# Kernel optimization log

Measured on AMD Instinct MI355X. Metric: run time of the kernel, lower is better.

## Reference

```python
import jax, jax.numpy as jnp
import numpy as np

N = 100000
E = 1600000
IN_DIM, HID, Z = 128, 64, 32


def gcn_conv(x, src, dst, num_nodes, W, b):
    """PyG GCNConv: add self-loops, symmetric deg^-1/2 normalization.
    x: [N, F_in]; src/dst: [E] int (self-loops already appended by caller wrapper).
    """
    h = x @ W  # [N, F_out] transform first (PyG order)
    ones = jnp.ones(src.shape[0], dtype=x.dtype)
    deg = jax.ops.segment_sum(ones, dst, num_segments=num_nodes)  # in-degree incl. self-loop
    dinv = jnp.where(deg > 0, jax.lax.rsqrt(deg), 0.0)
    norm = dinv[src] * dinv[dst]  # [E]
    msgs = h[src] * norm[:, None]  # [E, F_out] irregular gather
    out = jax.ops.segment_sum(msgs, dst, num_segments=num_nodes)  # scatter-add
    return out + b


def setup_inputs() -> dict:
    key = jax.random.key(0)
    ks = jax.random.split(key, 10)
    x = jax.random.normal(ks[0], (N, IN_DIM), dtype=jnp.float32)
    edge_index = jax.random.randint(ks[1], (2, E), 0, N, dtype=jnp.int64)

    def glorot(k, fan_in, fan_out):
        s = jnp.sqrt(6.0 / (fan_in + fan_out))
        return jax.random.uniform(k, (fan_in, fan_out), jnp.float32, -s, s)

    return {
        "x": x,
        "edge_index": edge_index,
        "W1": glorot(ks[2], IN_DIM, HID),
        "b1": jnp.zeros((HID,), jnp.float32),
        "W2": glorot(ks[3], HID, Z),
        "b2": jnp.zeros((Z,), jnp.float32),
        "Wmu": glorot(ks[4], Z, Z),
        "bmu": jnp.zeros((Z,), jnp.float32),
        "Wlv": glorot(ks[5], Z, Z),
        "blv": jnp.zeros((Z,), jnp.float32),
    }


def reference(x, edge_index, W1, b1, W2, b2, Wmu, bmu, Wlv, blv):
    num_nodes = x.shape[0]
    loop = jnp.arange(num_nodes, dtype=edge_index.dtype)
    src = jnp.concatenate([edge_index[0], loop])  # self-loops appended
    dst = jnp.concatenate([edge_index[1], loop])
    h = jax.nn.relu(gcn_conv(x, src, dst, num_nodes, W1, b1))
    h = gcn_conv(h, src, dst, num_nodes, W2, b2)
    mu = h @ Wmu + bmu
    logvar = h @ Wlv + blv
    return (mu, logvar)
```

## Files before the change

kernel.cpp:

```cpp
#include <hip/hip_runtime.h>

#define N_NODES 100000
#define N_EDGES 1600000
#define IN_F   128
#define HID_F  64
#define Z_F    32
#define NBUK   782
#define BCAP   3072
#define P1T    4096
#define P1_BLOCKS ((N_EDGES + P1T - 1) / P1T)
#define AGG_CAP 2048
#define G1_BLOCKS ((N_NODES + 63) / 64)

typedef unsigned int uint32;
typedef __attribute__((ext_vector_type(8))) short bf16x8;
typedef __attribute__((ext_vector_type(4))) float f32x4;

__device__ __forceinline__ unsigned short f2bf(float f) {
    unsigned u = __float_as_uint(f);
    u = (u + 0x7FFF + ((u >> 16) & 1)) >> 16;
    return (unsigned short)u;
}
__device__ __forceinline__ uint32 pack2bf(float lo, float hi) {
    return (uint32)f2bf(lo) | ((uint32)f2bf(hi) << 16);
}
__device__ __forceinline__ float bflo(uint32 u) { return __uint_as_float(u << 16); }
__device__ __forceinline__ float bfhi(uint32 u) { return __uint_as_float(u & 0xFFFF0000u); }

#define ACC8(u) { a0 += bflo(u.x); a1 += bfhi(u.x); a2 += bflo(u.y); a3 += bfhi(u.y); \
                  a4 += bflo(u.z); a5 += bfhi(u.z); a6 += bflo(u.w); a7 += bfhi(u.w); }

__global__ __launch_bounds__(512) void phase1_kernel(const int* __restrict__ ei,
                                                     int* __restrict__ gcur,
                                                     uint32* __restrict__ pairs,
                                                     const float* __restrict__ W1,
                                                     const float* __restrict__ W2,
                                                     const float* __restrict__ Wmu,
                                                     const float* __restrict__ Wlv,
                                                     unsigned short* __restrict__ Wt1,
                                                     unsigned short* __restrict__ Wt2,
                                                     unsigned short* __restrict__ Wth) {
    if (blockIdx.x == P1_BLOCKS) {
        int t = threadIdx.x;
        for (int i = t; i < IN_F * HID_F; i += 512) {
            int n = i >> 7, k = i & 127;
            Wt1[i] = f2bf(W1[k * HID_F + n]);
        }
        for (int i = t; i < HID_F * Z_F; i += 512) {
            int n = i >> 6, k = i & 63;
            Wt2[i] = f2bf(W2[k * Z_F + n]);
        }
        for (int i = t; i < Z_F * 64; i += 512) {
            int n = i >> 5, k = i & 31;
            Wth[i] = f2bf(n < 32 ? Wmu[k * Z_F + n] : Wlv[k * Z_F + (n - 32)]);
        }
        return;
    }
    __shared__ int hist[NBUK];
    __shared__ int lbase[NBUK];
    __shared__ int gbase[NBUK];
    __shared__ int lcur[NBUK];
    __shared__ uint32 stage[P1T];
    __shared__ unsigned short sbid[P1T];
    __shared__ int part[512];
    int tid = threadIdx.x;
    int e0 = blockIdx.x * P1T;
    int ecnt = N_EDGES - e0; if (ecnt > P1T) ecnt = P1T;
    for (int b = tid; b < NBUK; b += 512) { hist[b] = 0; lcur[b] = 0; }
    __syncthreads();
    int myd[8];
#pragma unroll
    for (int i = 0; i < 8; i++) {
        int k = tid + i * 512;
        myd[i] = (k < ecnt) ? ei[N_EDGES + e0 + k] : -1;
    }
#pragma unroll
    for (int i = 0; i < 8; i++)
        if (myd[i] >= 0) atomicAdd(&hist[myd[i] >> 7], 1);
    __syncthreads();
    int t2 = tid * 2;
    int l0 = 0, l1 = 0, s = 0;
    if (t2 + 0 < NBUK) { l0 = hist[t2 + 0]; s += l0; }
    if (t2 + 1 < NBUK) { l1 = hist[t2 + 1]; s += l1; }
    part[tid] = s;
    __syncthreads();
    for (int off = 1; off < 512; off <<= 1) {
        int add = (tid >= off) ? part[tid - off] : 0;
        __syncthreads();
        part[tid] += add;
        __syncthreads();
    }
    int run = part[tid] - s;
    if (t2 + 0 < NBUK) { lbase[t2 + 0] = run; run += l0; }
    if (t2 + 1 < NBUK) { lbase[t2 + 1] = run; }
    for (int b = tid; b < NBUK; b += 512) {
        int h = hist[b];
        gbase[b] = h ? atomicAdd(&gcur[b], h) : 0;
    }
    __syncthreads();
#pragma unroll
    for (int i = 0; i < 8; i++) {
        int k = tid + i * 512;
        if (k < ecnt) {
            int sN = ei[e0 + k];
            int d  = myd[i];
            int b = d >> 7;
            int slot = lbase[b] + atomicAdd(&lcur[b], 1);
            stage[slot] = (uint32)sN | ((uint32)(d & 127) << 17);
            sbid[slot] = (unsigned short)b;
        }
    }
    __syncthreads();
    for (int k = tid; k < ecnt; k += 512) {
        int b = sbid[k];
        int r = gbase[b] + (k - lbase[k < ecnt ? b : 0]);
        r = gbase[b] + (k - lbase[b]);
        if (r < BCAP) pairs[(size_t)b * BCAP + r] = stage[k];
    }
}

__global__ __launch_bounds__(256) void p2g1_kernel(const uint32* __restrict__ pairs,
                                                   const int* __restrict__ gcur,
                                                   int* __restrict__ rowptr,
                                                   float* __restrict__ dinv,
                                                   int* __restrict__ col,
                                                   const float* __restrict__ x,
                                                   const unsigned short* __restrict__ Wt1,
                                                   unsigned short* __restrict__ t1) {
    int tid = threadIdx.x;
    if (blockIdx.x < NBUK) {
        __shared__ int lhist[128];
        __shared__ int lscan[128];
        __shared__ int lcur[128];
        __shared__ int stage[BCAP];
        __shared__ int wsum[4];
        int b = blockIdx.x;
        int cnt_b = gcur[b];
        if (cnt_b > BCAP) cnt_b = BCAP;
        int partial = 0;
        for (int i = tid; i < b; i += 256) partial += gcur[i];
#pragma unroll
        for (int off = 32; off > 0; off >>= 1) partial += __shfl_down(partial, off);
        if (tid < 128) { lhist[tid] = 0; lcur[tid] = 0; }
        if ((tid & 63) == 0) wsum[tid >> 6] = partial;
        __syncthreads();
        int gbase = wsum[0] + wsum[1] + wsum[2] + wsum[3];
        int node0 = b << 7;
        int nb = N_NODES - node0;
        if (nb > 128) nb = 128;
        const uint32* pb = pairs + (size_t)b * BCAP;
        for (int k = tid; k < cnt_b; k += 256) atomicAdd(&lhist[pb[k] >> 17], 1);
        __syncthreads();
        int v = (tid < 128) ? lhist[tid] : 0;
        if (tid < 128) lscan[tid] = v;
        __syncthreads();
        for (int off = 1; off < 128; off <<= 1) {
            int add = (tid < 128 && tid >= off) ? lscan[tid - off] : 0;
            __syncthreads();
            if (tid < 128) lscan[tid] += add;
            __syncthreads();
        }
        if (tid < 128) lscan[tid] -= v;
        __syncthreads();
        if (tid < nb) {
            rowptr[node0 + tid] = gbase + lscan[tid];
            dinv[node0 + tid] = rsqrtf((float)(lhist[tid] + 1));
        }
        if (b == NBUK - 1 && tid == 0) rowptr[N_NODES] = N_EDGES;
        for (int k = tid; k < cnt_b; k += 256) {
            uint32 u = pb[k];
            int ld = u >> 17;
            int r = atomicAdd(&lcur[ld], 1);
            stage[lscan[ld] + r] = (int)(u & 0x1FFFF);
        }
        __syncthreads();
        for (int k = tid; k < cnt_b; k += 256) col[gbase + k] = stage[k];
        return;
    }
    __shared__ unsigned short Cs[64 * 72];
    __shared__ float dv[64];
    __shared__ int h64[64];
    int g = blockIdx.x - NBUK;
    int node0 = g * 64;
    int bk = node0 >> 7, half = (node0 >> 6) & 1;
    int cnt_b = gcur[bk];
    if (cnt_b > BCAP) cnt_b = BCAP;
    if (tid < 64) h64[tid] = 0;
    __syncthreads();
    const uint32* pb = pairs + (size_t)bk * BCAP;
    for (int k = tid; k < cnt_b; k += 256) {
        int ld = pb[k] >> 17;
        if ((ld >> 6) == half) atomicAdd(&h64[ld & 63], 1);
    }
    __syncthreads();
    if (tid < 64) {
        int n = node0 + tid;
        dv[tid] = (n < N_NODES) ? rsqrtf((float)(h64[tid] + 1)) : 0.f;
    }
    __syncthreads();
    int w = tid >> 6, lane = tid & 63;
    int m = lane & 15, quad = lane >> 4;
    int row = w * 16 + m;
    int node = node0 + row;
    const float* xr = x + (size_t)min(node, N_NODES - 1) * IN_F;
    f32x4 acc0 = {0.f, 0.f, 0.f, 0.f};
    f32x4 acc1 = acc0, acc2 = acc0, acc3 = acc0;
#pragma unroll
    for (int ks = 0; ks < 4; ks++) {
        int kb = ks * 32 + quad * 8;
        float4 f0 = *(const float4*)(xr + kb);
        float4 f1 = *(const float4*)(xr + kb + 4);
        union { bf16x8 v; unsigned short u[8]; } A;
        A.u[0] = f2bf(f0.x); A.u[1] = f2bf(f0.y); A.u[2] = f2bf(f0.z); A.u[3] = f2bf(f0.w);
        A.u[4] = f2bf(f1.x); A.u[5] = f2bf(f1.y); A.u[6] = f2bf(f1.z); A.u[7] = f2bf(f1.w);
        bf16x8 b0 = *(const bf16x8*)&Wt1[(0 * 16 + m) * IN_F + kb];
        bf16x8 b1 = *(const bf16x8*)&Wt1[(1 * 16 + m) * IN_F + kb];
        bf16x8 b2 = *(const bf16x8*)&Wt1[(2 * 16 + m) * IN_F + kb];
        bf16x8 b3 = *(const bf16x8*)&Wt1[(3 * 16 + m) * IN_F + kb];
        acc0 = __builtin_amdgcn_mfma_f32_16x16x32_bf16(A.v, b0, acc0, 0, 0, 0);
        acc1 = __builtin_amdgcn_mfma_f32_16x16x32_bf16(A.v, b1, acc1, 0, 0, 0);
        acc2 = __builtin_amdgcn_mfma_f32_16x16x32_bf16(A.v, b2, acc2, 0, 0, 0);
        acc3 = __builtin_amdgcn_mfma_f32_16x16x32_bf16(A.v, b3, acc3, 0, 0, 0);
    }
    int rbase = w * 16 + quad * 4;
#pragma unroll
    for (int reg = 0; reg < 4; reg++) {
        int r = rbase + reg;
        float d = dv[r];
        Cs[r * 72 +  0 + m] = f2bf(acc0[reg] * d);
        Cs[r * 72 + 16 + m] = f2bf(acc1[reg] * d);
        Cs[r * 72 + 32 + m] = f2bf(acc2[reg] * d);
        Cs[r * 72 + 48 + m] = f2bf(acc3[reg] * d);
    }
    __syncthreads();
#pragma unroll
    for (int it = 0; it < 4; it++) {
        int idx = it * 256 + tid;
        int r = idx >> 4, c = idx & 15;
        int nd = node0 + r;
        if (nd < N_NODES) {
            uint2 vv = *(const uint2*)&Cs[r * 72 + c * 4];
            *(uint2*)&t1[(size_t)nd * HID_F + c * 4] = vv;
        }
    }
}

__global__ __launch_bounds__(256) void agg1gemm2_kernel(const unsigned short* __restrict__ t1,
                                                        const int* __restrict__ rowptr,
                                                        const int* __restrict__ col,
                                                        const float* __restrict__ dinv,
                                                        const float* __restrict__ b1,
                                                        const unsigned short* __restrict__ Wt2,
                                                        unsigned short* __restrict__ t2s) {
    __shared__ int lcol[AGG_CAP];
    __shared__ int lrp[65];
    __shared__ float ldv[64];
    __shared__ unsigned short h1s[64 * 72];
    __shared__ unsigned short Cs[64 * 36];
    int tid = threadIdx.x;
    int node0 = blockIdx.x * 64;
    if (tid < 65) lrp[tid] = rowptr[min(node0 + tid, N_NODES)];
    __syncthreads();
    int s0 = lrp[0];
    int cnt = lrp[64] - s0; if (cnt > AGG_CAP) cnt = AGG_CAP;
    for (int k = tid; k < cnt; k += 256) lcol[k] = col[s0 + k];
    if (tid < 64) {
        int n = node0 + tid;
        ldv[tid] = (n < N_NODES) ? dinv[n] : 0.f;
    }
    __syncthreads();
    int lane = tid & 63, w = tid >> 6;
    int grp = lane >> 3, fl = lane & 7;
    int gg = w * 8 + grp;
    const uint4* t1q = (const uint4*)t1;
    float4 bb0 = ((const float4*)b1)[fl * 2];
    float4 bb1 = ((const float4*)b1)[fl * 2 + 1];
#pragma unroll
    for (int rep = 0; rep < 2; rep++) {
        int li = gg + rep * 32;
        int node = node0 + li;
        uint4 pk = make_uint4(0u, 0u, 0u, 0u);
        if (node < N_NODES) {
            int s = lrp[li] - s0;
            int e = lrp[li + 1] - s0; if (e > cnt) e = cnt;
            float a0 = 0.f, a1 = 0.f, a2 = 0.f, a3 = 0.f;
            float a4 = 0.f, a5 = 0.f, a6 = 0.f, a7 = 0.f;
            int p = s;
            for (; p + 3 < e; p += 4) {
                int c0 = lcol[p], c1 = lcol[p + 1], c2 = lcol[p + 2], c3 = lcol[p + 3];
                uint4 u0 = t1q[(size_t)c0 * 8 + fl];
                uint4 u1 = t1q[(size_t)c1 * 8 + fl];
                uint4 u2 = t1q[(size_t)c2 * 8 + fl];
                uint4 u3 = t1q[(size_t)c3 * 8 + fl];
                ACC8(u0); ACC8(u1); ACC8(u2); ACC8(u3);
            }
            for (; p < e; p++) {
                uint4 u = t1q[(size_t)lcol[p] * 8 + fl];
                ACC8(u);
            }
            uint4 us = t1q[(size_t)node * 8 + fl];
            float di = ldv[li];
            float o0 = fmaxf(di * (a0 + bflo(us.x)) + bb0.x, 0.f);
            float o1 = fmaxf(di * (a1 + bfhi(us.x)) + bb0.y, 0.f);
            float o2 = fmaxf(di * (a2 + bflo(us.y)) + bb0.z, 0.f);
            float o3 = fmaxf(di * (a3 + bfhi(us.y)) + bb0.w, 0.f);
            float o4 = fmaxf(di * (a4 + bflo(us.z)) + bb1.x, 0.f);
            float o5 = fmaxf(di * (a5 + bfhi(us.z)) + bb1.y, 0.f);
            float o6 = fmaxf(di * (a6 + bflo(us.w)) + bb1.z, 0.f);
            float o7 = fmaxf(di * (a7 + bfhi(us.w)) + bb1.w, 0.f);
            pk.x = pack2bf(o0, o1);
            pk.y = pack2bf(o2, o3);
            pk.z = pack2bf(o4, o5);
            pk.w = pack2bf(o6, o7);
        }
        *(uint4*)&h1s[li * 72 + fl * 8] = pk;
    }
    __syncthreads();
    int m = lane & 15, quad = lane >> 4;
    int row = w * 16 + m;
    f32x4 acc0 = {0.f, 0.f, 0.f, 0.f};
    f32x4 acc1 = acc0;
#pragma unroll
    for (int ks = 0; ks < 2; ks++) {
        int kb = ks * 32 + quad * 8;
        bf16x8 a  = *(const bf16x8*)&h1s[row * 72 + kb];
        bf16x8 b0 = *(const bf16x8*)&Wt2[(0 * 16 + m) * HID_F + kb];
        bf16x8 b1v = *(const bf16x8*)&Wt2[(1 * 16 + m) * HID_F + kb];
        acc0 = __builtin_amdgcn_mfma_f32_16x16x32_bf16(a, b0, acc0, 0, 0, 0);
        acc1 = __builtin_amdgcn_mfma_f32_16x16x32_bf16(a, b1v, acc1, 0, 0, 0);
    }
    int rbase = w * 16 + quad * 4;
#pragma unroll
    for (int reg = 0; reg < 4; reg++) {
        int r = rbase + reg;
        float d = ldv[r];
        Cs[r * 36 +  0 + m] = f2bf(acc0[reg] * d);
        Cs[r * 36 + 16 + m] = f2bf(acc1[reg] * d);
    }
    __syncthreads();
#pragma unroll
    for (int it = 0; it < 2; it++) {
        int idx = it * 256 + tid;
        int r = idx >> 3, c = idx & 7;
        int nd = node0 + r;
        if (nd < N_NODES) {
            uint2 vv = *(const uint2*)&Cs[r * 36 + c * 4];
            *(uint2*)&t2s[(size_t)nd * Z_F + c * 4] = vv;
        }
    }
}

__global__ __launch_bounds__(256) void agg2heads_kernel(const unsigned short* __restrict__ t2s,
                                                        const int* __restrict__ rowptr,
                                                        const int* __restrict__ col,
                                                        const float* __restrict__ dinv,
                                                        const float* __restrict__ b2,
                                                        const unsigned short* __restrict__ Wth,
                                                        const float* __restrict__ bmu,
                                                        const float* __restrict__ blv,
                                                        float* __restrict__ out) {
    __shared__ int lcol[AGG_CAP];
    __shared__ int lrp[65];
    __shared__ float ldv[64];
    __shared__ unsigned short h2s[64 * 40];
    __shared__ float Cf[64 * 68];
    __shared__ float bias[64];
    int tid = threadIdx.x;
    int node0 = blockIdx.x * 64;
    if (tid < 65) lrp[tid] = rowptr[min(node0 + tid, N_NODES)];
    else if (tid >= 96 && tid < 128) bias[tid - 96] = bmu[tid - 96];
    else if (tid >= 128 && tid < 160) bias[tid - 96] = blv[tid - 128];
    __syncthreads();
    int s0 = lrp[0];
    int cnt = lrp[64] - s0; if (cnt > AGG_CAP) cnt = AGG_CAP;
    for (int k = tid; k < cnt; k += 256) lcol[k] = col[s0 + k];
    if (tid < 64) {
        int n = node0 + tid;
        ldv[tid] = (n < N_NODES) ? dinv[n] : 0.f;
    }
    __syncthreads();
    int lane = tid & 63, w = tid >> 6;
    int grp = lane >> 2, fo = lane & 3;
    int li = w * 16 + grp;
    const uint4* t2q = (const uint4*)t2s;
    float4 bb0 = ((const float4*)b2)[fo * 2];
    float4 bb1 = ((const float4*)b2)[fo * 2 + 1];
    {
        int node = node0 + li;
        uint4 pk = make_uint4(0u, 0u, 0u, 0u);
        if (node < N_NODES) {
            int s = lrp[li] - s0;
            int e = lrp[li + 1] - s0; if (e > cnt) e = cnt;
            float a0 = 0.f, a1 = 0.f, a2 = 0.f, a3 = 0.f;
            float a4 = 0.f, a5 = 0.f, a6 = 0.f, a7 = 0.f;
            int p = s;
            for (; p + 3 < e; p += 4) {
                int c0 = lcol[p], c1 = lcol[p + 1], c2 = lcol[p + 2], c3 = lcol[p + 3];
                uint4 u0 = t2q[(size_t)c0 * 4 + fo];
                uint4 u1 = t2q[(size_t)c1 * 4 + fo];
                uint4 u2 = t2q[(size_t)c2 * 4 + fo];
                uint4 u3 = t2q[(size_t)c3 * 4 + fo];
                ACC8(u0); ACC8(u1); ACC8(u2); ACC8(u3);
            }
            for (; p < e; p++) {
                uint4 u = t2q[(size_t)lcol[p] * 4 + fo];
                ACC8(u);
            }
            uint4 us = t2q[(size_t)node * 4 + fo];
            float di = ldv[li];
            float o0 = di * (a0 + bflo(us.x)) + bb0.x;
            float o1 = di * (a1 + bfhi(us.x)) + bb0.y;
            float o2 = di * (a2 + bflo(us.y)) + bb0.z;
            float o3 = di * (a3 + bfhi(us.y)) + bb0.w;
            float o4 = di * (a4 + bflo(us.z)) + bb1.x;
            float o5 = di * (a5 + bfhi(us.z)) + bb1.y;
            float o6 = di * (a6 + bflo(us.w)) + bb1.z;
            float o7 = di * (a7 + bfhi(us.w)) + bb1.w;
            pk.x = pack2bf(o0, o1);
            pk.y = pack2bf(o2, o3);
            pk.z = pack2bf(o4, o5);
            pk.w = pack2bf(o6, o7);
        }
        *(uint4*)&h2s[li * 40 + fo * 8] = pk;
    }
    __syncthreads();
    int m = lane & 15, quad = lane >> 4;
    int row = w * 16 + m;
    int kb = quad * 8;
    bf16x8 a  = *(const bf16x8*)&h2s[row * 40 + kb];
    bf16x8 b0 = *(const bf16x8*)&Wth[(0 * 16 + m) * Z_F + kb];
    bf16x8 b1 = *(const bf16x8*)&Wth[(1 * 16 + m) * Z_F + kb];
    bf16x8 b2v = *(const bf16x8*)&Wth[(2 * 16 + m) * Z_F + kb];
    bf16x8 b3 = *(const bf16x8*)&Wth[(3 * 16 + m) * Z_F + kb];
    f32x4 acc0 = {0.f, 0.f, 0.f, 0.f};
    f32x4 acc1 = acc0, acc2 = acc0, acc3 = acc0;
    acc0 = __builtin_amdgcn_mfma_f32_16x16x32_bf16(a, b0, acc0, 0, 0, 0);
    acc1 = __builtin_amdgcn_mfma_f32_16x16x32_bf16(a, b1, acc1, 0, 0, 0);
    acc2 = __builtin_amdgcn_mfma_f32_16x16x32_bf16(a, b2v, acc2, 0, 0, 0);
    acc3 = __builtin_amdgcn_mfma_f32_16x16x32_bf16(a, b3, acc3, 0, 0, 0);
    int rbase = w * 16 + quad * 4;
#pragma unroll
    for (int reg = 0; reg < 4; reg++) {
        int r = rbase + reg;
        Cf[r * 68 +  0 + m] = acc0[reg] + bias[ 0 + m];
        Cf[r * 68 + 16 + m] = acc1[reg] + bias[16 + m];
        Cf[r * 68 + 32 + m] = acc2[reg] + bias[32 + m];
        Cf[r * 68 + 48 + m] = acc3[reg] + bias[48 + m];
    }
    __syncthreads();
#pragma unroll
    for (int it = 0; it < 2; it++) {
        int idx = it * 256 + tid;
        int r = idx >> 3, c = idx & 7;
        int nd = node0 + r;
        if (nd < N_NODES) {
            float4 vmu = *(const float4*)&Cf[r * 68 + c * 4];
            float4 vlv = *(const float4*)&Cf[r * 68 + 32 + c * 4];
            *(float4*)&out[(size_t)nd * Z_F + c * 4] = vmu;
            *(float4*)&out[(size_t)N_NODES * Z_F + (size_t)nd * Z_F + c * 4] = vlv;
        }
    }
}

extern "C" void kernel_launch(void* const* d_in, const int* in_sizes, int n_in,
                              void* d_out, int out_size, void* d_ws, size_t ws_size,
                              hipStream_t stream) {
    const float* x   = (const float*)d_in[0];
    const int*   ei  = (const int*)d_in[1];
    const float* W1  = (const float*)d_in[2];
    const float* b1  = (const float*)d_in[3];
    const float* W2  = (const float*)d_in[4];
    const float* b2  = (const float*)d_in[5];
    const float* Wmu = (const float*)d_in[6];
    const float* bmu = (const float*)d_in[7];
    const float* Wlv = (const float*)d_in[8];
    const float* blv = (const float*)d_in[9];
    float* out = (float*)d_out;

    char* ws = (char*)d_ws;
    size_t off = 0;
    auto A = [&](size_t bytes) {
        size_t r = off;
        off += (bytes + 255) & ~(size_t)255;
        return r;
    };
    int*   gcur   = (int*)(ws + A((size_t)NBUK * 4));
    int*   rowptr = (int*)(ws + A((size_t)(N_NODES + 1) * 4));
    float* dinv   = (float*)(ws + A((size_t)N_NODES * 4));
    unsigned short* Wt1 = (unsigned short*)(ws + A((size_t)IN_F * HID_F * 2));
    unsigned short* Wt2 = (unsigned short*)(ws + A((size_t)HID_F * Z_F * 2));
    unsigned short* Wth = (unsigned short*)(ws + A((size_t)Z_F * 64 * 2));
    int*   col        = (int*)(ws + A((size_t)N_EDGES * 4));
    char*  reg1 = ws + A((size_t)NBUK * BCAP * 4);
    uint32* pairs = (uint32*)reg1;
    unsigned short* t2s = (unsigned short*)reg1;
    unsigned short* t1 = (unsigned short*)(ws + A((size_t)N_NODES * HID_F * 2));

    hipMemsetAsync(gcur, 0, (size_t)NBUK * 4, stream);

    phase1_kernel<<<P1_BLOCKS + 1, 512, 0, stream>>>(ei, gcur, pairs,
                                                     W1, W2, Wmu, Wlv, Wt1, Wt2, Wth);
    p2g1_kernel<<<NBUK + G1_BLOCKS, 256, 0, stream>>>(pairs, gcur, rowptr, dinv, col,
                                                      x, Wt1, t1);
    agg1gemm2_kernel<<<G1_BLOCKS, 256, 0, stream>>>(t1, rowptr, col, dinv, b1, Wt2, t2s);
    agg2heads_kernel<<<G1_BLOCKS, 256, 0, stream>>>(t2s, rowptr, col, dinv, b2, Wth, bmu, blv, out);
}
```

Measured before the change: 210.6 us.

## Fuse bucketing with GEMM1, drop CSR build, aggregate directly from bucket pairs

```diff
diff --git a/kernel.cpp b/kernel.cpp
--- a/kernel.cpp
+++ b/kernel.cpp
@@ -9,8 +9,7 @@
 #define BCAP   3072
 #define P1T    4096
 #define P1_BLOCKS ((N_EDGES + P1T - 1) / P1T)
-#define AGG_CAP 2048
-#define G1_BLOCKS ((N_NODES + 63) / 64)
+#define DEG_PAD 100352
 
 typedef unsigned int uint32;
 typedef __attribute__((ext_vector_type(8))) short bf16x8;
@@ -29,175 +28,109 @@
 
 #define ACC8(u) { a0 += bflo(u.x); a1 += bfhi(u.x); a2 += bflo(u.y); a3 += bfhi(u.y); \
                   a4 += bflo(u.z); a5 += bfhi(u.z); a6 += bflo(u.w); a7 += bfhi(u.w); }
-
-__global__ __launch_bounds__(512) void phase1_kernel(const int* __restrict__ ei,
-                                                     int* __restrict__ gcur,
-                                                     uint32* __restrict__ pairs,
-                                                     const float* __restrict__ W1,
-                                                     const float* __restrict__ W2,
-                                                     const float* __restrict__ Wmu,
-                                                     const float* __restrict__ Wlv,
-                                                     unsigned short* __restrict__ Wt1,
-                                                     unsigned short* __restrict__ Wt2,
-                                                     unsigned short* __restrict__ Wth) {
+#define FMA8(r,u) { a0 = fmaf(r, bflo(u.x), a0); a1 = fmaf(r, bfhi(u.x), a1); \
+                    a2 = fmaf(r, bflo(u.y), a2); a3 = fmaf(r, bfhi(u.y), a3); \
+                    a4 = fmaf(r, bflo(u.z), a4); a5 = fmaf(r, bfhi(u.z), a5); \
+                    a6 = fmaf(r, bflo(u.w), a6); a7 = fmaf(r, bfhi(u.w), a7); }
+
+__global__ __launch_bounds__(512) void k1_kernel(const int* __restrict__ ei,
+                                                 int* __restrict__ gcur,
+                                                 uint32* __restrict__ pairs,
+                                                 int* __restrict__ deg,
+                                                 const float* __restrict__ W1,
+                                                 const float* __restrict__ W2,
+                                                 const float* __restrict__ Wmu,
+                                                 const float* __restrict__ Wlv,
+                                                 unsigned short* __restrict__ Wt2,
+                                                 unsigned short* __restrict__ Wth,
+                                                 const float* __restrict__ x,
+                                                 unsigned short* __restrict__ t1u) {
+    __shared__ __align__(16) int arena[9784];
+    int tid = threadIdx.x;
     if (blockIdx.x == P1_BLOCKS) {
-        int t = threadIdx.x;
-        for (int i = t; i < IN_F * HID_F; i += 512) {
-            int n = i >> 7, k = i & 127;
-            Wt1[i] = f2bf(W1[k * HID_F + n]);
-        }
-        for (int i = t; i < HID_F * Z_F; i += 512) {
+        for (int i = tid; i < HID_F * Z_F; i += 512) {
             int n = i >> 6, k = i & 63;
             Wt2[i] = f2bf(W2[k * Z_F + n]);
         }
-        for (int i = t; i < Z_F * 64; i += 512) {
+        for (int i = tid; i < Z_F * 64; i += 512) {
             int n = i >> 5, k = i & 31;
             Wth[i] = f2bf(n < 32 ? Wmu[k * Z_F + n] : Wlv[k * Z_F + (n - 32)]);
         }
         return;
     }
-    __shared__ int hist[NBUK];
-    __shared__ int lbase[NBUK];
-    __shared__ int gbase[NBUK];
-    __shared__ int lcur[NBUK];
-    __shared__ uint32 stage[P1T];
-    __shared__ unsigned short sbid[P1T];
-    __shared__ int part[512];
-    int tid = threadIdx.x;
-    int e0 = blockIdx.x * P1T;
-    int ecnt = N_EDGES - e0; if (ecnt > P1T) ecnt = P1T;
-    for (int b = tid; b < NBUK; b += 512) { hist[b] = 0; lcur[b] = 0; }
-    __syncthreads();
-    int myd[8];
-#pragma unroll
-    for (int i = 0; i < 8; i++) {
-        int k = tid + i * 512;
-        myd[i] = (k < ecnt) ? ei[N_EDGES + e0 + k] : -1;
-    }
-#pragma unroll
-    for (int i = 0; i < 8; i++)
-        if (myd[i] >= 0) atomicAdd(&hist[myd[i] >> 7], 1);
-    __syncthreads();
-    int t2 = tid * 2;
-    int l0 = 0, l1 = 0, s = 0;
-    if (t2 + 0 < NBUK) { l0 = hist[t2 + 0]; s += l0; }
-    if (t2 + 1 < NBUK) { l1 = hist[t2 + 1]; s += l1; }
-    part[tid] = s;
-    __syncthreads();
-    for (int off = 1; off < 512; off <<= 1) {
-        int add = (tid >= off) ? part[tid - off] : 0;
-        __syncthreads();
-        part[tid] += add;
-        __syncthreads();
-    }
-    int run = part[tid] - s;
-    if (t2 + 0 < NBUK) { lbase[t2 + 0] = run; run += l0; }
-    if (t2 + 1 < NBUK) { lbase[t2 + 1] = run; }
-    for (int b = tid; b < NBUK; b += 512) {
-        int h = hist[b];
-        gbase[b] = h ? atomicAdd(&gcur[b], h) : 0;
-    }
-    __syncthreads();
-#pragma unroll
-    for (int i = 0; i < 8; i++) {
-        int k = tid + i * 512;
-        if (k < ecnt) {
-            int sN = ei[e0 + k];
-            int d  = myd[i];
-            int b = d >> 7;
-            int slot = lbase[b] + atomicAdd(&lcur[b], 1);
-            stage[slot] = (uint32)sN | ((uint32)(d & 127) << 17);
-            sbid[slot] = (unsigned short)b;
-        }
-    }
-    __syncthreads();
-    for (int k = tid; k < ecnt; k += 512) {
-        int b = sbid[k];
-        int r = gbase[b] + (k - lbase[k < ecnt ? b : 0]);
-        r = gbase[b] + (k - lbase[b]);
-        if (r < BCAP) pairs[(size_t)b * BCAP + r] = stage[k];
-    }
-}
-
-__global__ __launch_bounds__(256) void p2g1_kernel(const uint32* __restrict__ pairs,
-                                                   const int* __restrict__ gcur,
-                                                   int* __restrict__ rowptr,
-                                                   float* __restrict__ dinv,
-                                                   int* __restrict__ col,
-                                                   const float* __restrict__ x,
-                                                   const unsigned short* __restrict__ Wt1,
-                                                   unsigned short* __restrict__ t1) {
-    int tid = threadIdx.x;
-    if (blockIdx.x < NBUK) {
-        __shared__ int lhist[128];
-        __shared__ int lscan[128];
-        __shared__ int lcur[128];
-        __shared__ int stage[BCAP];
-        __shared__ int wsum[4];
-        int b = blockIdx.x;
-        int cnt_b = gcur[b];
-        if (cnt_b > BCAP) cnt_b = BCAP;
-        int partial = 0;
-        for (int i = tid; i < b; i += 256) partial += gcur[i];
-#pragma unroll
-        for (int off = 32; off > 0; off >>= 1) partial += __shfl_down(partial, off);
-        if (tid < 128) { lhist[tid] = 0; lcur[tid] = 0; }
-        if ((tid & 63) == 0) wsum[tid >> 6] = partial;
-        __syncthreads();
-        int gbase = wsum[0] + wsum[1] + wsum[2] + wsum[3];
-        int node0 = b << 7;
-        int nb = N_NODES - node0;
-        if (nb > 128) nb = 128;
-        const uint32* pb = pairs + (size_t)b * BCAP;
-        for (int k = tid; k < cnt_b; k += 256) atomicAdd(&lhist[pb[k] >> 17], 1);
-        __syncthreads();
-        int v = (tid < 128) ? lhist[tid] : 0;
-        if (tid < 128) lscan[tid] = v;
-        __syncthreads();
-        for (int off = 1; off < 128; off <<= 1) {
-            int add = (tid < 128 && tid >= off) ? lscan[tid - off] : 0;
+    if (blockIdx.x < P1_BLOCKS) {
+        int* hist  = arena;
+        int* lbase = arena + NBUK;
+        int* gbase = arena + 2 * NBUK;
+        int* lcur  = arena + 3 * NBUK;
+        int* part  = arena + 4 * NBUK;
+        uint32* stage = (uint32*)(arena + 4 * NBUK + 512);
+        unsigned short* sbid = (unsigned short*)(arena + 4 * NBUK + 512 + P1T);
+        int e0 = blockIdx.x * P1T;
+        int ecnt = N_EDGES - e0; if (ecnt > P1T) ecnt = P1T;
+        for (int b = tid; b < NBUK; b += 512) { hist[b] = 0; lcur[b] = 0; }
+        __syncthreads();
+        int myd[8];
+#pragma unroll
+        for (int i = 0; i < 8; i++) {
+            int k = tid + i * 512;
+            myd[i] = (k < ecnt) ? ei[N_EDGES + e0 + k] : -1;
+        }
+#pragma unroll
+        for (int i = 0; i < 8; i++)
+            if (myd[i] >= 0) {
+                atomicAdd(&hist[myd[i] >> 7], 1);
+                atomicAdd(&deg[myd[i]], 1);
+            }
+        __syncthreads();
+        int t2 = tid * 2;
+        int l0 = 0, l1 = 0, s = 0;
+        if (t2 + 0 < NBUK) { l0 = hist[t2 + 0]; s += l0; }
+        if (t2 + 1 < NBUK) { l1 = hist[t2 + 1]; s += l1; }
+        part[tid] = s;
+        __syncthreads();
+        for (int off = 1; off < 512; off <<= 1) {
+            int add = (tid >= off) ? part[tid - off] : 0;
             __syncthreads();
-            if (tid < 128) lscan[tid] += add;
+            part[tid] += add;
             __syncthreads();
         }
-        if (tid < 128) lscan[tid] -= v;
-        __syncthreads();
-        if (tid < nb) {
-            rowptr[node0 + tid] = gbase + lscan[tid];
-            dinv[node0 + tid] = rsqrtf((float)(lhist[tid] + 1));
-        }
-        if (b == NBUK - 1 && tid == 0) rowptr[N_NODES] = N_EDGES;
-        for (int k = tid; k < cnt_b; k += 256) {
-            uint32 u = pb[k];
-            int ld = u >> 17;
-            int r = atomicAdd(&lcur[ld], 1);
-            stage[lscan[ld] + r] = (int)(u & 0x1FFFF);
-        }
-        __syncthreads();
-        for (int k = tid; k < cnt_b; k += 256) col[gbase + k] = stage[k];
+        int run = part[tid] - s;
+        if (t2 + 0 < NBUK) { lbase[t2 + 0] = run; run += l0; }
+        if (t2 + 1 < NBUK) { lbase[t2 + 1] = run; }
+        for (int b = tid; b < NBUK; b += 512) {
+            int h = hist[b];
+            gbase[b] = h ? atomicAdd(&gcur[b], h) : 0;
+        }
+        __syncthreads();
+#pragma unroll
+        for (int i = 0; i < 8; i++) {
+            int k = tid + i * 512;
+            if (k < ecnt) {
+                int sN = ei[e0 + k];
+                int d  = myd[i];
+                int b = d >> 7;
+                int slot = lbase[b] + atomicAdd(&lcur[b], 1);
+                stage[slot] = (uint32)sN | ((uint32)(d & 127) << 17);
+                sbid[slot] = (unsigned short)b;
+            }
+        }
+        __syncthreads();
+        for (int k = tid; k < ecnt; k += 512) {
+            int b = sbid[k];
+            int r = gbase[b] + (k - lbase[b]);
+            if (r < BCAP) pairs[(size_t)b * BCAP + r] = stage[k];
+        }
         return;
     }
-    __shared__ unsigned short Cs[64 * 72];
-    __shared__ float dv[64];
-    __shared__ int h64[64];
-    int g = blockIdx.x - NBUK;
-    int node0 = g * 64;
-    int bk = node0 >> 7, half = (node0 >> 6) & 1;
-    int cnt_b = gcur[bk];
-    if (cnt_b > BCAP) cnt_b = BCAP;
-    if (tid < 64) h64[tid] = 0;
-    __syncthreads();
-    const uint32* pb = pairs + (size_t)bk * BCAP;
-    for (int k = tid; k < cnt_b; k += 256) {
-        int ld = pb[k] >> 17;
-        if ((ld >> 6) == half) atomicAdd(&h64[ld & 63], 1);
-    }
-    __syncthreads();
-    if (tid < 64) {
-        int n = node0 + tid;
-        dv[tid] = (n < N_NODES) ? rsqrtf((float)(h64[tid] + 1)) : 0.f;
-    }
-    __syncthreads();
+    unsigned short* Cs   = (unsigned short*)arena;
+    unsigned short* Wt1s = (unsigned short*)(arena + 4608);
+    for (int i = tid; i < IN_F * HID_F; i += 512) {
+        int k = i >> 6, n = i & 63;
+        Wt1s[n * 132 + k] = f2bf(W1[i]);
+    }
+    __syncthreads();
+    int node0 = (blockIdx.x - P1_BLOCKS - 1) * 128;
     int w = tid >> 6, lane = tid & 63;
     int m = lane & 15, quad = lane >> 4;
     int row = w * 16 + m;
@@ -213,10 +146,10 @@
         union { bf16x8 v; unsigned short u[8]; } A;
         A.u[0] = f2bf(f0.x); A.u[1] = f2bf(f0.y); A.u[2] = f2bf(f0.z); A.u[3] = f2bf(f0.w);
         A.u[4] = f2bf(f1.x); A.u[5] = f2bf(f1.y); A.u[6] = f2bf(f1.z); A.u[7] = f2bf(f1.w);
-        bf16x8 b0 = *(const bf16x8*)&Wt1[(0 * 16 + m) * IN_F + kb];
-        bf16x8 b1 = *(const bf16x8*)&Wt1[(1 * 16 + m) * IN_F + kb];
-        bf16x8 b2 = *(const bf16x8*)&Wt1[(2 * 16 + m) * IN_F + kb];
-        bf16x8 b3 = *(const bf16x8*)&Wt1[(3 * 16 + m) * IN_F + kb];
+        bf16x8 b0 = *(const bf16x8*)&Wt1s[(0 * 16 + m) * 132 + kb];
+        bf16x8 b1 = *(const bf16x8*)&Wt1s[(1 * 16 + m) * 132 + kb];
+        bf16x8 b2 = *(const bf16x8*)&Wt1s[(2 * 16 + m) * 132 + kb];
+        bf16x8 b3 = *(const bf16x8*)&Wt1s[(3 * 16 + m) * 132 + kb];
         acc0 = __builtin_amdgcn_mfma_f32_16x16x32_bf16(A.v, b0, acc0, 0, 0, 0);
         acc1 = __builtin_amdgcn_mfma_f32_16x16x32_bf16(A.v, b1, acc1, 0, 0, 0);
         acc2 = __builtin_amdgcn_mfma_f32_16x16x32_bf16(A.v, b2, acc2, 0, 0, 0);
@@ -226,63 +159,81 @@
 #pragma unroll
     for (int reg = 0; reg < 4; reg++) {
         int r = rbase + reg;
-        float d = dv[r];
-        Cs[r * 72 +  0 + m] = f2bf(acc0[reg] * d);
-        Cs[r * 72 + 16 + m] = f2bf(acc1[reg] * d);
-        Cs[r * 72 + 32 + m] = f2bf(acc2[reg] * d);
-        Cs[r * 72 + 48 + m] = f2bf(acc3[reg] * d);
+        Cs[r * 72 +  0 + m] = f2bf(acc0[reg]);
+        Cs[r * 72 + 16 + m] = f2bf(acc1[reg]);
+        Cs[r * 72 + 32 + m] = f2bf(acc2[reg]);
+        Cs[r * 72 + 48 + m] = f2bf(acc3[reg]);
     }
     __syncthreads();
 #pragma unroll
     for (int it = 0; it < 4; it++) {
-        int idx = it * 256 + tid;
+        int idx = it * 512 + tid;
         int r = idx >> 4, c = idx & 15;
         int nd = node0 + r;
         if (nd < N_NODES) {
             uint2 vv = *(const uint2*)&Cs[r * 72 + c * 4];
-            *(uint2*)&t1[(size_t)nd * HID_F + c * 4] = vv;
-        }
-    }
-}
-
-__global__ __launch_bounds__(256) void agg1gemm2_kernel(const unsigned short* __restrict__ t1,
-                                                        const int* __restrict__ rowptr,
-                                                        const int* __restrict__ col,
-                                                        const float* __restrict__ dinv,
+            *(uint2*)&t1u[(size_t)nd * HID_F + c * 4] = vv;
+        }
+    }
+}
+
+__global__ __launch_bounds__(512) void agg1gemm2_kernel(const unsigned short* __restrict__ t1u,
+                                                        const uint32* __restrict__ pairs,
+                                                        const int* __restrict__ gcur,
+                                                        const int* __restrict__ deg,
                                                         const float* __restrict__ b1,
                                                         const unsigned short* __restrict__ Wt2,
                                                         unsigned short* __restrict__ t2s) {
-    __shared__ int lcol[AGG_CAP];
-    __shared__ int lrp[65];
-    __shared__ float ldv[64];
-    __shared__ unsigned short h1s[64 * 72];
-    __shared__ unsigned short Cs[64 * 36];
+    __shared__ __align__(16) int arena[BCAP + 128 * 72 / 2];
+    __shared__ int lhist[128];
+    __shared__ int lscan[128];
+    __shared__ int lcur[128];
+    __shared__ float dv[128];
+    int* lcol = arena;
+    unsigned short* h1s = (unsigned short*)(arena + BCAP);
+    unsigned short* Cs  = (unsigned short*)arena;
     int tid = threadIdx.x;
-    int node0 = blockIdx.x * 64;
-    if (tid < 65) lrp[tid] = rowptr[min(node0 + tid, N_NODES)];
-    __syncthreads();
-    int s0 = lrp[0];
-    int cnt = lrp[64] - s0; if (cnt > AGG_CAP) cnt = AGG_CAP;
-    for (int k = tid; k < cnt; k += 256) lcol[k] = col[s0 + k];
-    if (tid < 64) {
-        int n = node0 + tid;
-        ldv[tid] = (n < N_NODES) ? dinv[n] : 0.f;
+    int b = blockIdx.x;
+    int node0 = b << 7;
+    int cnt = gcur[b]; if (cnt > BCAP) cnt = BCAP;
+    const uint32* pb = pairs + (size_t)b * BCAP;
+    if (tid < 128) { lhist[tid] = 0; lcur[tid] = 0; }
+    __syncthreads();
+    for (int k = tid; k < cnt; k += 512) atomicAdd(&lhist[pb[k] >> 17], 1);
+    __syncthreads();
+    int v = (tid < 128) ? lhist[tid] : 0;
+    if (tid < 128) lscan[tid] = v;
+    __syncthreads();
+    for (int off = 1; off < 128; off <<= 1) {
+        int add = (tid < 128 && tid >= off) ? lscan[tid - off] : 0;
+        __syncthreads();
+        if (tid < 128) lscan[tid] += add;
+        __syncthreads();
+    }
+    if (tid < 128) lscan[tid] -= v;
+    __syncthreads();
+    if (tid < 128) dv[tid] = (node0 + tid < N_NODES) ? rsqrtf((float)(lhist[tid] + 1)) : 0.f;
+    for (int k = tid; k < cnt; k += 512) {
+        uint32 u = pb[k];
+        int ld = u >> 17;
+        int r = atomicAdd(&lcur[ld], 1);
+        lcol[lscan[ld] + r] = (int)(u & 0x1FFFF);
     }
     __syncthreads();
     int lane = tid & 63, w = tid >> 6;
     int grp = lane >> 3, fl = lane & 7;
     int gg = w * 8 + grp;
-    const uint4* t1q = (const uint4*)t1;
+    const uint4* t1q = (const uint4*)t1u;
     float4 bb0 = ((const float4*)b1)[fl * 2];
     float4 bb1 = ((const float4*)b1)[fl * 2 + 1];
 #pragma unroll
     for (int rep = 0; rep < 2; rep++) {
-        int li = gg + rep * 32;
+        int li = gg + rep * 64;
         int node = node0 + li;
         uint4 pk = make_uint4(0u, 0u, 0u, 0u);
         if (node < N_NODES) {
-            int s = lrp[li] - s0;
-            int e = lrp[li + 1] - s0; if (e > cnt) e = cnt;
+            int s = lscan[li];
+            int e = s + lhist[li];
             float a0 = 0.f, a1 = 0.f, a2 = 0.f, a3 = 0.f;
             float a4 = 0.f, a5 = 0.f, a6 = 0.f, a7 = 0.f;
             int p = s;
@@ -292,22 +243,29 @@
                 uint4 u1 = t1q[(size_t)c1 * 8 + fl];
                 uint4 u2 = t1q[(size_t)c2 * 8 + fl];
                 uint4 u3 = t1q[(size_t)c3 * 8 + fl];
-                ACC8(u0); ACC8(u1); ACC8(u2); ACC8(u3);
+                int d0 = deg[c0], d1 = deg[c1], d2 = deg[c2], d3 = deg[c3];
+                float r0 = rsqrtf((float)(d0 + 1));
+                float r1 = rsqrtf((float)(d1 + 1));
+                float r2 = rsqrtf((float)(d2 + 1));
+                float r3 = rsqrtf((float)(d3 + 1));
+                FMA8(r0, u0); FMA8(r1, u1); FMA8(r2, u2); FMA8(r3, u3);
             }
             for (; p < e; p++) {
-                uint4 u = t1q[(size_t)lcol[p] * 8 + fl];
-                ACC8(u);
+                int c = lcol[p];
+                uint4 u = t1q[(size_t)c * 8 + fl];
+                float r = rsqrtf((float)(deg[c] + 1));
+                FMA8(r, u);
             }
             uint4 us = t1q[(size_t)node * 8 + fl];
-            float di = ldv[li];
-            float o0 = fmaxf(di * (a0 + bflo(us.x)) + bb0.x, 0.f);
-            float o1 = fmaxf(di * (a1 + bfhi(us.x)) + bb0.y, 0.f);
-            float o2 = fmaxf(di * (a2 + bflo(us.y)) + bb0.z, 0.f);
-            float o3 = fmaxf(di * (a3 + bfhi(us.y)) + bb0.w, 0.f);
-            float o4 = fmaxf(di * (a4 + bflo(us.z)) + bb1.x, 0.f);
-            float o5 = fmaxf(di * (a5 + bfhi(us.z)) + bb1.y, 0.f);
-            float o6 = fmaxf(di * (a6 + bflo(us.w)) + bb1.z, 0.f);
-            float o7 = fmaxf(di * (a7 + bfhi(us.w)) + bb1.w, 0.f);
+            float dvl = dv[li];
+            float o0 = fmaxf(fmaf(dvl, fmaf(dvl, bflo(us.x), a0), bb0.x), 0.f);
+            float o1 = fmaxf(fmaf(dvl, fmaf(dvl, bfhi(us.x), a1), bb0.y), 0.f);
+            float o2 = fmaxf(fmaf(dvl, fmaf(dvl, bflo(us.y), a2), bb0.z), 0.f);
+            float o3 = fmaxf(fmaf(dvl, fmaf(dvl, bfhi(us.y), a3), bb0.w), 0.f);
+            float o4 = fmaxf(fmaf(dvl, fmaf(dvl, bflo(us.z), a4), bb1.x), 0.f);
+            float o5 = fmaxf(fmaf(dvl, fmaf(dvl, bfhi(us.z), a5), bb1.y), 0.f);
+            float o6 = fmaxf(fmaf(dvl, fmaf(dvl, bflo(us.w), a6), bb1.z), 0.f);
+            float o7 = fmaxf(fmaf(dvl, fmaf(dvl, bfhi(us.w), a7), bb1.w), 0.f);
             pk.x = pack2bf(o0, o1);
             pk.y = pack2bf(o2, o3);
             pk.z = pack2bf(o4, o5);
@@ -324,23 +282,23 @@
     for (int ks = 0; ks < 2; ks++) {
         int kb = ks * 32 + quad * 8;
         bf16x8 a  = *(const bf16x8*)&h1s[row * 72 + kb];
-        bf16x8 b0 = *(const bf16x8*)&Wt2[(0 * 16 + m) * HID_F + kb];
-        bf16x8 b1v = *(const bf16x8*)&Wt2[(1 * 16 + m) * HID_F + kb];
-        acc0 = __builtin_amdgcn_mfma_f32_16x16x32_bf16(a, b0, acc0, 0, 0, 0);
-        acc1 = __builtin_amdgcn_mfma_f32_16x16x32_bf16(a, b1v, acc1, 0, 0, 0);
+        bf16x8 B0 = *(const bf16x8*)&Wt2[(0 * 16 + m) * HID_F + kb];
+        bf16x8 B1 = *(const bf16x8*)&Wt2[(1 * 16 + m) * HID_F + kb];
+        acc0 = __builtin_amdgcn_mfma_f32_16x16x32_bf16(a, B0, acc0, 0, 0, 0);
+        acc1 = __builtin_amdgcn_mfma_f32_16x16x32_bf16(a, B1, acc1, 0, 0, 0);
     }
     int rbase = w * 16 + quad * 4;
 #pragma unroll
     for (int reg = 0; reg < 4; reg++) {
         int r = rbase + reg;
-        float d = ldv[r];
+        float d = dv[r];
         Cs[r * 36 +  0 + m] = f2bf(acc0[reg] * d);
         Cs[r * 36 + 16 + m] = f2bf(acc1[reg] * d);
     }
     __syncthreads();
 #pragma unroll
     for (int it = 0; it < 2; it++) {
-        int idx = it * 256 + tid;
+        int idx = it * 512 + tid;
         int r = idx >> 3, c = idx & 7;
         int nd = node0 + r;
         if (nd < N_NODES) {
@@ -350,33 +308,51 @@
     }
 }
 
-__global__ __launch_bounds__(256) void agg2heads_kernel(const unsigned short* __restrict__ t2s,
-                                                        const int* __restrict__ rowptr,
-                                                        const int* __restrict__ col,
-                                                        const float* __restrict__ dinv,
+__global__ __launch_bounds__(512) void agg2heads_kernel(const unsigned short* __restrict__ t2s,
+                                                        const uint32* __restrict__ pairs,
+                                                        const int* __restrict__ gcur,
                                                         const float* __restrict__ b2,
                                                         const unsigned short* __restrict__ Wth,
                                                         const float* __restrict__ bmu,
                                                         const float* __restrict__ blv,
                                                         float* __restrict__ out) {
-    __shared__ int lcol[AGG_CAP];
-    __shared__ int lrp[65];
-    __shared__ float ldv[64];
-    __shared__ unsigned short h2s[64 * 40];
-    __shared__ float Cf[64 * 68];
+    __shared__ __align__(16) int arena[BCAP + 128 * 40 / 2];
+    __shared__ int lhist[128];
+    __shared__ int lscan[128];
+    __shared__ int lcur[128];
+    __shared__ float dv[128];
     __shared__ float bias[64];
+    int* lcol = arena;
+    unsigned short* h2s = (unsigned short*)(arena + BCAP);
+    float* Cf = (float*)arena;
     int tid = threadIdx.x;
-    int node0 = blockIdx.x * 64;
-    if (tid < 65) lrp[tid] = rowptr[min(node0 + tid, N_NODES)];
-    else if (tid >= 96 && tid < 128) bias[tid - 96] = bmu[tid - 96];
-    else if (tid >= 128 && tid < 160) bias[tid - 96] = blv[tid - 128];
-    __syncthreads();
-    int s0 = lrp[0];
-    int cnt = lrp[64] - s0; if (cnt > AGG_CAP) cnt = AGG_CAP;
-    for (int k = tid; k < cnt; k += 256) lcol[k] = col[s0 + k];
-    if (tid < 64) {
-        int n = node0 + tid;
-        ldv[tid] = (n < N_NODES) ? dinv[n] : 0.f;
+    int b = blockIdx.x;
+    int node0 = b << 7;
+    int cnt = gcur[b]; if (cnt > BCAP) cnt = BCAP;
+    const uint32* pb = pairs + (size_t)b * BCAP;
+    if (tid < 128) { lhist[tid] = 0; lcur[tid] = 0; }
+    if (tid >= 256 && tid < 288) bias[tid - 256] = bmu[tid - 256];
+    if (tid >= 288 && tid < 320) bias[tid - 288 + 32] = blv[tid - 288];
+    __syncthreads();
+    for (int k = tid; k < cnt; k += 512) atomicAdd(&lhist[pb[k] >> 17], 1);
+    __syncthreads();
+    int v = (tid < 128) ? lhist[tid] : 0;
+    if (tid < 128) lscan[tid] = v;
+    __syncthreads();
+    for (int off = 1; off < 128; off <<= 1) {
+        int add = (tid < 128 && tid >= off) ? lscan[tid - off] : 0;
+        __syncthreads();
+        if (tid < 128) lscan[tid] += add;
+        __syncthreads();
+    }
+    if (tid < 128) lscan[tid] -= v;
+    __syncthreads();
+    if (tid < 128) dv[tid] = (node0 + tid < N_NODES) ? rsqrtf((float)(lhist[tid] + 1)) : 0.f;
+    for (int k = tid; k < cnt; k += 512) {
+        uint32 u = pb[k];
+        int ld = u >> 17;
+        int r = atomicAdd(&lcur[ld], 1);
+        lcol[lscan[ld] + r] = (int)(u & 0x1FFFF);
     }
     __syncthreads();
     int lane = tid & 63, w = tid >> 6;
@@ -389,8 +365,8 @@
         int node = node0 + li;
         uint4 pk = make_uint4(0u, 0u, 0u, 0u);
         if (node < N_NODES) {
-            int s = lrp[li] - s0;
-            int e = lrp[li + 1] - s0; if (e > cnt) e = cnt;
+            int s = lscan[li];
+            int e = s + lhist[li];
             float a0 = 0.f, a1 = 0.f, a2 = 0.f, a3 = 0.f;
             float a4 = 0.f, a5 = 0.f, a6 = 0.f, a7 = 0.f;
             int p = s;
@@ -407,7 +383,7 @@
                 ACC8(u);
             }
             uint4 us = t2q[(size_t)node * 4 + fo];
-            float di = ldv[li];
+            float di = dv[li];
             float o0 = di * (a0 + bflo(us.x)) + bb0.x;
             float o1 = di * (a1 + bfhi(us.x)) + bb0.y;
             float o2 = di * (a2 + bflo(us.y)) + bb0.z;
@@ -428,37 +404,43 @@
     int row = w * 16 + m;
     int kb = quad * 8;
     bf16x8 a  = *(const bf16x8*)&h2s[row * 40 + kb];
-    bf16x8 b0 = *(const bf16x8*)&Wth[(0 * 16 + m) * Z_F + kb];
-    bf16x8 b1 = *(const bf16x8*)&Wth[(1 * 16 + m) * Z_F + kb];
-    bf16x8 b2v = *(const bf16x8*)&Wth[(2 * 16 + m) * Z_F + kb];
-    bf16x8 b3 = *(const bf16x8*)&Wth[(3 * 16 + m) * Z_F + kb];
+    bf16x8 B0 = *(const bf16x8*)&Wth[(0 * 16 + m) * Z_F + kb];
+    bf16x8 B1 = *(const bf16x8*)&Wth[(1 * 16 + m) * Z_F + kb];
+    bf16x8 B2 = *(const bf16x8*)&Wth[(2 * 16 + m) * Z_F + kb];
+    bf16x8 B3 = *(const bf16x8*)&Wth[(3 * 16 + m) * Z_F + kb];
     f32x4 acc0 = {0.f, 0.f, 0.f, 0.f};
     f32x4 acc1 = acc0, acc2 = acc0, acc3 = acc0;
-    acc0 = __builtin_amdgcn_mfma_f32_16x16x32_bf16(a, b0, acc0, 0, 0, 0);
-    acc1 = __builtin_amdgcn_mfma_f32_16x16x32_bf16(a, b1, acc1, 0, 0, 0);
-    acc2 = __builtin_amdgcn_mfma_f32_16x16x32_bf16(a, b2v, acc2, 0, 0, 0);
-    acc3 = __builtin_amdgcn_mfma_f32_16x16x32_bf16(a, b3, acc3, 0, 0, 0);
-    int rbase = w * 16 + quad * 4;
-#pragma unroll
-    for (int reg = 0; reg < 4; reg++) {
-        int r = rbase + reg;
-        Cf[r * 68 +  0 + m] = acc0[reg] + bias[ 0 + m];
-        Cf[r * 68 + 16 + m] = acc1[reg] + bias[16 + m];
-        Cf[r * 68 + 32 + m] = acc2[reg] + bias[32 + m];
-        Cf[r * 68 + 48 + m] = acc3[reg] + bias[48 + m];
-    }
-    __syncthreads();
-#pragma unroll
-    for (int it = 0; it < 2; it++) {
-        int idx = it * 256 + tid;
-        int r = idx >> 3, c = idx & 7;
-        int nd = node0 + r;
-        if (nd < N_NODES) {
-            float4 vmu = *(const float4*)&Cf[r * 68 + c * 4];
-            float4 vlv = *(const float4*)&Cf[r * 68 + 32 + c * 4];
-            *(float4*)&out[(size_t)nd * Z_F + c * 4] = vmu;
-            *(float4*)&out[(size_t)N_NODES * Z_F + (size_t)nd * Z_F + c * 4] = vlv;
-        }
+    acc0 = __builtin_amdgcn_mfma_f32_16x16x32_bf16(a, B0, acc0, 0, 0, 0);
+    acc1 = __builtin_amdgcn_mfma_f32_16x16x32_bf16(a, B1, acc1, 0, 0, 0);
+    acc2 = __builtin_amdgcn_mfma_f32_16x16x32_bf16(a, B2, acc2, 0, 0, 0);
+    acc3 = __builtin_amdgcn_mfma_f32_16x16x32_bf16(a, B3, acc3, 0, 0, 0);
+    __syncthreads();
+    float* outlv = out + (size_t)N_NODES * Z_F;
+#pragma unroll
+    for (int h = 0; h < 2; h++) {
+        if ((w >> 2) == h) {
+            int r2 = (w & 3) * 16 + quad * 4;
+#pragma unroll
+            for (int reg = 0; reg < 4; reg++) {
+                int rr = r2 + reg;
+                Cf[rr * 68 +  0 + m] = acc0[reg] + bias[ 0 + m];
+                Cf[rr * 68 + 16 + m] = acc1[reg] + bias[16 + m];
+                Cf[rr * 68 + 32 + m] = acc2[reg] + bias[32 + m];
+                Cf[rr * 68 + 48 + m] = acc3[reg] + bias[48 + m];
+            }
+        }
+        __syncthreads();
+        {
+            int r2 = tid >> 3, c = tid & 7;
+            int nd = node0 + h * 64 + r2;
+            if (nd < N_NODES) {
+                float4 vmu = *(const float4*)&Cf[r2 * 68 + c * 4];
+                float4 vlv = *(const float4*)&Cf[r2 * 68 + 32 + c * 4];
+                *(float4*)&out[(size_t)nd * Z_F + c * 4] = vmu;
+                *(float4*)&outlv[(size_t)nd * Z_F + c * 4] = vlv;
+            }
+        }
+        __syncthreads();
     }
 }
 
@@ -484,24 +466,19 @@
         off += (bytes + 255) & ~(size_t)255;
         return r;
     };
-    int*   gcur   = (int*)(ws + A((size_t)NBUK * 4));
-    int*   rowptr = (int*)(ws + A((size_t)(N_NODES + 1) * 4));
-    float* dinv   = (float*)(ws + A((size_t)N_NODES * 4));
-    unsigned short* Wt1 = (unsigned short*)(ws + A((size_t)IN_F * HID_F * 2));
+    int*   deg  = (int*)(ws + A((size_t)DEG_PAD * 4));
+    int*   gcur = (int*)(ws + A((size_t)NBUK * 4));
     unsigned short* Wt2 = (unsigned short*)(ws + A((size_t)HID_F * Z_F * 2));
     unsigned short* Wth = (unsigned short*)(ws + A((size_t)Z_F * 64 * 2));
-    int*   col        = (int*)(ws + A((size_t)N_EDGES * 4));
-    char*  reg1 = ws + A((size_t)NBUK * BCAP * 4);
-    uint32* pairs = (uint32*)reg1;
-    unsigned short* t2s = (unsigned short*)reg1;
-    unsigned short* t1 = (unsigned short*)(ws + A((size_t)N_NODES * HID_F * 2));
-
-    hipMemsetAsync(gcur, 0, (size_t)NBUK * 4, stream);
-
-    phase1_kernel<<<P1_BLOCKS + 1, 512, 0, stream>>>(ei, gcur, pairs,
-                                                     W1, W2, Wmu, Wlv, Wt1, Wt2, Wth);
-    p2g1_kernel<<<NBUK + G1_BLOCKS, 256, 0, stream>>>(pairs, gcur, rowptr, dinv, col,
-                                                      x, Wt1, t1);
-    agg1gemm2_kernel<<<G1_BLOCKS, 256, 0, stream>>>(t1, rowptr, col, dinv, b1, Wt2, t2s);
-    agg2heads_kernel<<<G1_BLOCKS, 256, 0, stream>>>(t2s, rowptr, col, dinv, b2, Wth, bmu, blv, out);
-}
+    uint32* pairs = (uint32*)(ws + A((size_t)NBUK * BCAP * 4));
+    unsigned short* t1u = (unsigned short*)(ws + A((size_t)N_NODES * HID_F * 2));
+    unsigned short* t2s = (unsigned short*)(ws + A((size_t)N_NODES * Z_F * 2));
+
+    hipMemsetAsync(deg, 0, (size_t)DEG_PAD * 4 + (size_t)NBUK * 4, stream);
+
+    k1_kernel<<<P1_BLOCKS + 1 + NBUK, 512, 0, stream>>>(ei, gcur, pairs, deg,
+                                                        W1, W2, Wmu, Wlv, Wt2, Wth,
+                                                        x, t1u);
+    agg1gemm2_kernel<<<NBUK, 512, 0, stream>>>(t1u, pairs, gcur, deg, b1, Wt2, t2s);
+    agg2heads_kernel<<<NBUK, 512, 0, stream>>>(t2s, pairs, gcur, b2, Wth, bmu, blv, out);
+}
```

Result: slower. 256.5 us (+21.8%).
